# Performance work log

Measured on AMD Instinct MI355X. Metric: run time of the kernel, lower is better.

## Reference

```python
import jax, jax.numpy as jnp
import numpy as np

DIM = 256
HEADS = 8
B, T, D, H, W = 2, 8, 16, 16, 16


def _mha(x, wqkv, bqkv, wo, bo):
    # x: [M, S, F]; standard self-attention (q=k=v=x), LoRA rank 0.
    M, S, F = x.shape
    hd = F // HEADS
    qkv = jnp.einsum('msf,kfg->kmsg', x, wqkv) + bqkv[:, None, None, :]  # [3,M,S,F]
    q, k, v = qkv
    q = q.reshape(M, S, HEADS, hd).transpose(0, 2, 1, 3)  # [M,Hh,S,hd]
    k = k.reshape(M, S, HEADS, hd).transpose(0, 2, 1, 3)
    v = v.reshape(M, S, HEADS, hd).transpose(0, 2, 1, 3)
    scores = jnp.einsum('mhsd,mhtd->mhst', q, k) / jnp.sqrt(jnp.asarray(hd, x.dtype))
    attn = jax.nn.softmax(scores, axis=-1)
    out = jnp.einsum('mhst,mhtd->mhsd', attn, v)
    out = out.transpose(0, 2, 1, 3).reshape(M, S, F)
    return out @ wo + bo


def _make_params(key, name_suffix):
    k1, k2 = jax.random.split(key)
    s = 1.0 / np.sqrt(DIM)
    return {
        f'wqkv_{name_suffix}': jax.random.normal(k1, (3, DIM, DIM), jnp.float32) * s,
        f'bqkv_{name_suffix}': jnp.zeros((3, DIM), jnp.float32),
        f'wo_{name_suffix}': jax.random.normal(k2, (DIM, DIM), jnp.float32) * s,
        f'bo_{name_suffix}': jnp.zeros((DIM,), jnp.float32),
    }


def setup_inputs() -> dict:
    key = jax.random.key(0)
    ks = jax.random.split(key, 5)
    inp = {'x': jax.random.normal(ks[0], (B, T, D * H * W, DIM), jnp.float32)}
    for k, ax in zip(ks[1:], ['t', 'd', 'h', 'w']):
        inp.update(_make_params(k, ax))
    inp['grid_d'] = D
    inp['grid_h'] = H
    inp['grid_w'] = W
    return inp


def reference(x, wqkv_t, bqkv_t, wo_t, bo_t,
              wqkv_d, bqkv_d, wo_d, bo_d,
              wqkv_h, bqkv_h, wo_h, bo_h,
              wqkv_w, bqkv_w, wo_w, bo_w,
              grid_d, grid_h, grid_w):
    b, t, n, f = x.shape
    d, h, w = grid_d, grid_h, grid_w
    x = x.reshape(b, t, d, h, w, f)
    if t > 1:
        xt = x.transpose(0, 2, 3, 4, 1, 5).reshape(b * d * h * w, t, f)
        xt = _mha(xt, wqkv_t, bqkv_t, wo_t, bo_t)
        xt = xt.reshape(b, d, h, w, t, f).transpose(0, 4, 1, 2, 3, 5)
        x = x + xt
    xd = x.transpose(0, 1, 3, 4, 2, 5).reshape(b * t * h * w, d, f)
    xd = _mha(xd, wqkv_d, bqkv_d, wo_d, bo_d)
    xd = xd.reshape(b, t, h, w, d, f).transpose(0, 1, 4, 2, 3, 5)
    xh = x.transpose(0, 1, 2, 4, 3, 5).reshape(b * t * d * w, h, f)
    xh = _mha(xh, wqkv_h, bqkv_h, wo_h, bo_h)
    xh = xh.reshape(b, t, d, w, h, f).transpose(0, 1, 2, 4, 3, 5)
    xw = x.reshape(b * t * d * h, w, f)
    xw = _mha(xw, wqkv_w, bqkv_w, wo_w, bo_w)
    xw = xw.reshape(b, t, d, h, w, f)
    x_comb = x + xd + xh + xw
    return x_comb.reshape(b, t, d * h * w, f)
```

## Files before the change

### kernel.cpp

```cpp
#include <hip/hip_runtime.h>

typedef __attribute__((ext_vector_type(4))) float f32x4;
typedef __attribute__((ext_vector_type(8))) short s16x8;

__device__ __forceinline__ ushort f2bf(float f) {
  union { float f; uint u; } v; v.f = f;
  uint r = v.u + 0x7fffu + ((v.u >> 16) & 1u);
  return (ushort)(r >> 16);
}

__device__ __forceinline__ void glds16(const void* g, void* l) {
  __builtin_amdgcn_global_load_lds(
      (const __attribute__((address_space(1))) uint*)g,
      (__attribute__((address_space(3))) uint*)l, 16, 0, 0);
}

__device__ __forceinline__ int asidx(int row, int col) {
  return row*256 + ((((col>>3) ^ (row & 7)))<<3) + (col&7);
}
__device__ __forceinline__ int scridx(int row, int col) {
  return row*32 + ((((col>>3) ^ ((row>>2)&3)))<<3) + (col&7);
}
__device__ __forceinline__ int epidx(int row, int f) {
  return row*256 + (f ^ ((row & 7) << 2));
}

struct WSrc { const float* p[8]; };

__global__ __launch_bounds__(256) void prep_weights(WSrc s, ushort* wq, ushort* wo) {
  int mm = blockIdx.x >> 6;
  int t  = blockIdx.x & 63;
  int a = mm >> 2, sub = mm & 3;
  const float* src = (sub < 3) ? (s.p[a*2] + sub*65536) : s.p[a*2+1];
  ushort*      dst = (sub < 3) ? (wq + (a*3 + sub)*65536) : (wo + a*65536);
  int gt = (t >> 3) * 32, ft = (t & 7) * 32;
  __shared__ float tile[32][33];
  int lx = threadIdx.x & 31, ly = threadIdx.x >> 5;
#pragma unroll
  for (int i = 0; i < 4; i++)
    tile[ly + i*8][lx] = src[(ft + ly + i*8)*256 + gt + lx];
  __syncthreads();
#pragma unroll
  for (int i = 0; i < 4; i++) {
    int n = gt + ly + i*8, col = ft + lx;
    dst[asidx(n, col)] = f2bf(tile[lx][ly + i*8]);
  }
}

template<int AXIS>
__device__ __forceinline__ int token_index(int blk, int row) {
  if (AXIS == 0) {
    int seq = blk*8 + (row >> 3);
    int t = row & 7;
    int b = seq >> 12, n = seq & 4095;
    return (b*8 + t)*4096 + n;
  } else {
    int sid = blk*4 + (row >> 4);
    int bt = sid >> 8, lo = sid & 255, r = row & 15;
    if (AXIS == 1) { int hh = lo >> 4, ww = lo & 15; return bt*4096 + r*256 + hh*16 + ww; }
    if (AXIS == 2) { int dd = lo >> 4, ww = lo & 15; return bt*4096 + dd*256 + r*16 + ww; }
    { int dd = lo >> 4, hh = lo & 15; return bt*4096 + dd*256 + hh*16 + r; }
  }
}

#define PUB_BARRIER() do { \
    __builtin_amdgcn_sched_barrier(0); \
    asm volatile("s_waitcnt lgkmcnt(0)" ::: "memory"); \
    __builtin_amdgcn_sched_barrier(0); \
    __builtin_amdgcn_s_barrier(); \
    __builtin_amdgcn_sched_barrier(0); } while (0)

template<int AXIS>
__global__ __launch_bounds__(512, 4) void axial_pass(
    const float* __restrict__ x0, const ushort* __restrict__ xb,
    const ushort* __restrict__ wqkvT, const float* __restrict__ bqkv,
    const ushort* __restrict__ woT, const float* __restrict__ bo,
    float* __restrict__ out, ushort* __restrict__ x1b) {

  __shared__ ushort smem[40960];
  ushort* Wb0 = smem;
  ushort* Wb1 = smem + 8192;
  ushort* As  = smem + 16384;
  ushort* ScrB = smem + 32768;

  const int tid = threadIdx.x, blk = blockIdx.x;
  const int wv = tid >> 6, lane = tid & 63, llo = lane & 15, lhi = lane >> 4;
  const int pr = wv >> 1, half = wv & 1;
  const int rr = half*16 + llo;
  ushort* Qs = ScrB + pr*2048;
  ushort* Ks = Qs + 512;
  ushort* Vt = Qs + 1024;
  const f32x4 fzero = {0.f, 0.f, 0.f, 0.f};
  const s16x8 szero = {0,0,0,0,0,0,0,0};

  auto issue_stage = [&](int s) {
    const ushort* src = (s < 24) ? (wqkvT + (s % 3)*65536 + (s / 3)*8192)
                                 : (woT + (s - 24)*8192);
    const ushort* g = src + wv*1024 + lane*8;
    ushort* l = ((s & 1) ? Wb1 : Wb0) + wv*1024;
    glds16(g, l);
    glds16(g + 512, l + 512);
  };

#define STAGE_SYNC(sn) do { \
    __builtin_amdgcn_sched_barrier(0); \
    asm volatile("s_waitcnt vmcnt(0) lgkmcnt(0)" ::: "memory"); \
    __builtin_amdgcn_sched_barrier(0); \
    __builtin_amdgcn_s_barrier(); \
    __builtin_amdgcn_sched_barrier(0); \
    if ((sn) < 32) issue_stage(sn); \
  } while (0)

  issue_stage(0);

  {
    int row = tid >> 3, j = tid & 7;
    int tok = token_index<AXIS>(blk, row);
    if (AXIS == 0) {
      const float4* s4 = (const float4*)(x0 + (size_t)tok*256);
#pragma unroll
      for (int i = 0; i < 4; i++) {
        int c = j + 8*i;
        float4 v0 = s4[c*2], v1 = s4[c*2 + 1];
        s16x8 o;
        o[0] = (short)f2bf(v0.x); o[1] = (short)f2bf(v0.y);
        o[2] = (short)f2bf(v0.z); o[3] = (short)f2bf(v0.w);
        o[4] = (short)f2bf(v1.x); o[5] = (short)f2bf(v1.y);
        o[6] = (short)f2bf(v1.z); o[7] = (short)f2bf(v1.w);
        *(s16x8*)(As + asidx(row, c*8)) = o;
      }
    } else {
      const s16x8* s8 = (const s16x8*)(xb + (size_t)tok*256);
#pragma unroll
      for (int i = 0; i < 4; i++) {
        int c = j + 8*i;
        *(s16x8*)(As + asidx(row, c*8)) = s8[c];
      }
    }
  }
  {
    int row = half*16 + (lane >> 2);
    int cc = 2 + (lane & 1);
    *(s16x8*)(Vt + row*32 + ((cc ^ ((row>>2)&3))<<3)) = szero;
  }
  __syncthreads();

  s16x8 af[8];
  const int xrow = pr*16 + llo;
#pragma unroll
  for (int ks = 0; ks < 8; ks++)
    af[ks] = *(const s16x8*)(As + asidx(xrow, (ks*4 + lhi)*8));

  auto proj = [&](int sb) -> f32x4 {
    const ushort* buf = sb ? Wb1 : Wb0;
    f32x4 ca = fzero, cb = fzero;
    __builtin_amdgcn_s_setprio(1);
#pragma unroll
    for (int ks = 0; ks < 4; ks++) {
      s16x8 b0 = *(const s16x8*)(buf + asidx(rr, (ks*4 + lhi)*8));
      s16x8 b1 = *(const s16x8*)(buf + asidx(rr, ((ks+4)*4 + lhi)*8));
      ca = __builtin_amdgcn_mfma_f32_16x16x32_bf16(af[ks],   b0, ca, 0, 0, 0);
      cb = __builtin_amdgcn_mfma_f32_16x16x32_bf16(af[ks+4], b1, cb, 0, 0, 0);
    }
    __builtin_amdgcn_s_setprio(0);
    return ca + cb;
  };

#pragma unroll 1
  for (int h = 0; h < 8; h++) {
    STAGE_SYNC(3*h + 1);
    {
      f32x4 c = proj((3*h) & 1);
      float bias = bqkv[0*256 + h*32 + rr];
#pragma unroll
      for (int r = 0; r < 4; r++)
        Qs[scridx(lhi*4 + r, rr)] = f2bf(c[r] + bias);
    }
    STAGE_SYNC(3*h + 2);
    {
      f32x4 c = proj((3*h + 1) & 1);
      float bias = bqkv[1*256 + h*32 + rr];
#pragma unroll
      for (int r = 0; r < 4; r++)
        Ks[scridx(lhi*4 + r, rr)] = f2bf(c[r] + bias);
    }
    STAGE_SYNC(3*h + 3);
    {
      f32x4 c = proj((3*h + 2) & 1);
      float bias = bqkv[2*256 + h*32 + rr];
#pragma unroll
      for (int r = 0; r < 4; r++)
        Vt[scridx(rr, lhi*4 + r)] = f2bf(c[r] + bias);

      s16x8 aq = *(const s16x8*)(Qs + scridx(llo, lhi*8));
      s16x8 bk = *(const s16x8*)(Ks + scridx(llo, lhi*8));
      f32x4 sc = __builtin_amdgcn_mfma_f32_16x16x32_bf16(aq, bk, fzero, 0, 0, 0);

      PUB_BARRIER();

#pragma unroll
      for (int r = 0; r < 4; r++) {
        float s = sc[r] * 0.17677669529663689f;
        if (AXIS == 0) {
          int srow = lhi*4 + r;
          if ((srow >> 3) != (llo >> 3)) s = -1e30f;
        }
        float mx = s;
        mx = fmaxf(mx, __shfl_xor(mx, 1));
        mx = fmaxf(mx, __shfl_xor(mx, 2));
        mx = fmaxf(mx, __shfl_xor(mx, 4));
        mx = fmaxf(mx, __shfl_xor(mx, 8));
        float e = __expf(s - mx);
        float sm = e;
        sm += __shfl_xor(sm, 1);
        sm += __shfl_xor(sm, 2);
        sm += __shfl_xor(sm, 4);
        sm += __shfl_xor(sm, 8);
        Ks[scridx(lhi*4 + r, llo)] = f2bf(e * __builtin_amdgcn_rcpf(sm));
      }
      s16x8 ap = *(const s16x8*)(Ks + scridx(llo, lhi*8));
      s16x8 bv = *(const s16x8*)(Vt + scridx(rr, lhi*8));
      f32x4 o = __builtin_amdgcn_mfma_f32_16x16x32_bf16(ap, bv, fzero, 0, 0, 0);
#pragma unroll
      for (int r = 0; r < 4; r++)
        As[asidx(pr*16 + lhi*4 + r, h*32 + rr)] = f2bf(o[r]);
    }
  }

  f32x4 acc[8];
#pragma unroll 1
  for (int st = 0; st < 8; st++) {
    STAGE_SYNC(25 + st);
    if (st == 0) {
#pragma unroll
      for (int ks = 0; ks < 8; ks++)
        af[ks] = *(const s16x8*)(As + asidx(xrow, (ks*4 + lhi)*8));
#pragma unroll
      for (int i = 0; i < 8; i++) acc[i] = fzero;
    }
    {
      const ushort* buf = (st & 1) ? Wb1 : Wb0;
      f32x4 t0 = fzero;
      __builtin_amdgcn_s_setprio(1);
#pragma unroll
      for (int ks = 0; ks < 4; ks++) {
        s16x8 b0 = *(const s16x8*)(buf + asidx(rr, (ks*4 + lhi)*8));
        s16x8 b1 = *(const s16x8*)(buf + asidx(rr, ((ks+4)*4 + lhi)*8));
        acc[st] = __builtin_amdgcn_mfma_f32_16x16x32_bf16(af[ks],   b0, acc[st], 0, 0, 0);
        t0      = __builtin_amdgcn_mfma_f32_16x16x32_bf16(af[ks+4], b1, t0,      0, 0, 0);
      }
      __builtin_amdgcn_s_setprio(0);
      acc[st] = acc[st] + t0;
    }
  }

  float* Fep = (float*)smem;
  PUB_BARRIER();
#pragma unroll
  for (int st = 0; st < 8; st++) {
#pragma unroll
    for (int r = 0; r < 4; r++) {
      int row = pr*16 + lhi*4 + r;
      Fep[epidx(row, st*32 + half*16 + llo)] = acc[st][r];
    }
  }
  PUB_BARRIER();
  {
    int row = tid >> 3, g = tid & 7;
    int tok = token_index<AXIS>(blk, row);
    size_t base = (size_t)tok*256;
#pragma unroll
    for (int i = 0; i < 8; i++) {
      int f = i*32 + g*4;
      float4 v = *(float4*)&Fep[epidx(row, f)];
      float4 b = *(const float4*)&bo[f];
      v.x += b.x; v.y += b.y; v.z += b.z; v.w += b.w;
      if (AXIS == 0) {
        float4 x = *(const float4*)&x0[base + f];
        v.x += x.x; v.y += x.y; v.z += x.z; v.w += x.w;
        *(float4*)&out[base + f] = v;
        ushort4 p; p.x = f2bf(v.x); p.y = f2bf(v.y);
        p.z = f2bf(v.z); p.w = f2bf(v.w);
        *(ushort4*)&x1b[base + f] = p;
      } else {
        float4 o = *(float4*)&out[base + f];
        o.x += v.x; o.y += v.y; o.z += v.z; o.w += v.w;
        *(float4*)&out[base + f] = o;
      }
    }
  }
#undef STAGE_SYNC
}

extern "C" void kernel_launch(void* const* d_in, const int* in_sizes, int n_in,
                              void* d_out, int out_size, void* d_ws, size_t ws_size,
                              hipStream_t stream) {
  const float* x = (const float*)d_in[0];
  ushort* wq  = (ushort*)d_ws;
  ushort* wo  = wq + 4*3*65536;
  ushort* x1b = wo + 4*65536;
  float* out = (float*)d_out;

  WSrc wsrc;
  wsrc.p[0] = (const float*)d_in[1];  wsrc.p[1] = (const float*)d_in[3];
  wsrc.p[2] = (const float*)d_in[5];  wsrc.p[3] = (const float*)d_in[7];
  wsrc.p[4] = (const float*)d_in[9];  wsrc.p[5] = (const float*)d_in[11];
  wsrc.p[6] = (const float*)d_in[13]; wsrc.p[7] = (const float*)d_in[15];
  prep_weights<<<dim3(1024), dim3(256), 0, stream>>>(wsrc, wq, wo);

  const float* bq_t = (const float*)d_in[2];  const float* bo_t = (const float*)d_in[4];
  const float* bq_d = (const float*)d_in[6];  const float* bo_d = (const float*)d_in[8];
  const float* bq_h = (const float*)d_in[10]; const float* bo_h = (const float*)d_in[12];
  const float* bq_w = (const float*)d_in[14]; const float* bo_w = (const float*)d_in[16];

  axial_pass<0><<<dim3(1024), dim3(512), 0, stream>>>(x, nullptr, wq + 0*3*65536, bq_t, wo + 0*65536, bo_t, out, x1b);
  axial_pass<1><<<dim3(1024), dim3(512), 0, stream>>>(nullptr, x1b, wq + 1*3*65536, bq_d, wo + 1*65536, bo_d, out, nullptr);
  axial_pass<2><<<dim3(1024), dim3(512), 0, stream>>>(nullptr, x1b, wq + 2*3*65536, bq_h, wo + 2*65536, bo_h, out, nullptr);
  axial_pass<3><<<dim3(1024), dim3(512), 0, stream>>>(nullptr, x1b, wq + 3*3*65536, bq_w, wo + 3*65536, bo_w, out, nullptr);
}
```

Baseline: 402.8 us.

## Halve block to 256 threads, each wave computing two row groups

```diff
diff --git a/kernel.cpp b/kernel.cpp
--- a/kernel.cpp
+++ b/kernel.cpp
@@ -71,7 +71,7 @@
     __builtin_amdgcn_sched_barrier(0); } while (0)
 
 template<int AXIS>
-__global__ __launch_bounds__(512, 4) void axial_pass(
+__global__ __launch_bounds__(256, 2) void axial_pass(
     const float* __restrict__ x0, const ushort* __restrict__ xb,
     const ushort* __restrict__ wqkvT, const float* __restrict__ bqkv,
     const ushort* __restrict__ woT, const float* __restrict__ bo,
@@ -80,26 +80,22 @@
   __shared__ ushort smem[40960];
   ushort* Wb0 = smem;
   ushort* Wb1 = smem + 8192;
-  ushort* As  = smem + 16384;
-  ushort* ScrB = smem + 32768;
+  ushort* AsT = smem + 16384;
+  ushort* Scr = smem + 32768;
 
   const int tid = threadIdx.x, blk = blockIdx.x;
   const int wv = tid >> 6, lane = tid & 63, llo = lane & 15, lhi = lane >> 4;
-  const int pr = wv >> 1, half = wv & 1;
-  const int rr = half*16 + llo;
-  ushort* Qs = ScrB + pr*2048;
-  ushort* Ks = Qs + 512;
-  ushort* Vt = Qs + 1024;
+  const int rg = wv >> 1, ch = wv & 1;
   const f32x4 fzero = {0.f, 0.f, 0.f, 0.f};
   const s16x8 szero = {0,0,0,0,0,0,0,0};
 
   auto issue_stage = [&](int s) {
     const ushort* src = (s < 24) ? (wqkvT + (s % 3)*65536 + (s / 3)*8192)
                                  : (woT + (s - 24)*8192);
-    const ushort* g = src + wv*1024 + lane*8;
-    ushort* l = ((s & 1) ? Wb1 : Wb0) + wv*1024;
-    glds16(g, l);
-    glds16(g + 512, l + 512);
+    const ushort* g = src + wv*2048 + lane*8;
+    ushort* l = ((s & 1) ? Wb1 : Wb0) + wv*2048;
+#pragma unroll
+    for (int i = 0; i < 4; i++) glds16(g + i*512, l + i*512);
   };
 
 #define STAGE_SYNC(sn) do { \
@@ -114,144 +110,156 @@
   issue_stage(0);
 
   {
-    int row = tid >> 3, j = tid & 7;
+    int row = tid >> 2, q = tid & 3;
     int tok = token_index<AXIS>(blk, row);
     if (AXIS == 0) {
-      const float4* s4 = (const float4*)(x0 + (size_t)tok*256);
-#pragma unroll
-      for (int i = 0; i < 4; i++) {
-        int c = j + 8*i;
-        float4 v0 = s4[c*2], v1 = s4[c*2 + 1];
+      const float4* s4 = (const float4*)(x0 + (size_t)tok*256 + q*64);
+#pragma unroll
+      for (int c2 = 0; c2 < 8; c2++) {
+        float4 v0 = s4[c2*2], v1 = s4[c2*2 + 1];
         s16x8 o;
         o[0] = (short)f2bf(v0.x); o[1] = (short)f2bf(v0.y);
         o[2] = (short)f2bf(v0.z); o[3] = (short)f2bf(v0.w);
         o[4] = (short)f2bf(v1.x); o[5] = (short)f2bf(v1.y);
         o[6] = (short)f2bf(v1.z); o[7] = (short)f2bf(v1.w);
-        *(s16x8*)(As + asidx(row, c*8)) = o;
+        *(s16x8*)(AsT + asidx(row, (q*8 + c2)*8)) = o;
       }
     } else {
-      const s16x8* s8 = (const s16x8*)(xb + (size_t)tok*256);
-#pragma unroll
-      for (int i = 0; i < 4; i++) {
-        int c = j + 8*i;
-        *(s16x8*)(As + asidx(row, c*8)) = s8[c];
-      }
+      const s16x8* s8 = (const s16x8*)(xb + (size_t)tok*256 + q*64);
+#pragma unroll
+      for (int c2 = 0; c2 < 8; c2++)
+        *(s16x8*)(AsT + asidx(row, (q*8 + c2)*8)) = s8[c2];
     }
   }
   {
-    int row = half*16 + (lane >> 2);
-    int cc = 2 + (lane & 1);
-    *(s16x8*)(Vt + row*32 + ((cc ^ ((row>>2)&3))<<3)) = szero;
+    ushort* Vtw = Scr + wv*2048 + 1024;
+    *(s16x8*)(Vtw + scridx(lane >> 1, 16 + (lane & 1)*8)) = szero;
   }
   __syncthreads();
 
-  s16x8 af[8];
-  const int xrow = pr*16 + llo;
-#pragma unroll
-  for (int ks = 0; ks < 8; ks++)
-    af[ks] = *(const s16x8*)(As + asidx(xrow, (ks*4 + lhi)*8));
-
-  auto proj = [&](int sb) -> f32x4 {
+  s16x8 af[2][8];
+#pragma unroll
+  for (int g = 0; g < 2; g++)
+#pragma unroll
+    for (int ks = 0; ks < 8; ks++)
+      af[g][ks] = *(const s16x8*)(AsT + asidx(rg*32 + g*16 + llo, (ks*4 + lhi)*8));
+
+  auto proj2 = [&](int sb, f32x4& c0, f32x4& c1) {
     const ushort* buf = sb ? Wb1 : Wb0;
-    f32x4 ca = fzero, cb = fzero;
     __builtin_amdgcn_s_setprio(1);
 #pragma unroll
-    for (int ks = 0; ks < 4; ks++) {
-      s16x8 b0 = *(const s16x8*)(buf + asidx(rr, (ks*4 + lhi)*8));
-      s16x8 b1 = *(const s16x8*)(buf + asidx(rr, ((ks+4)*4 + lhi)*8));
-      ca = __builtin_amdgcn_mfma_f32_16x16x32_bf16(af[ks],   b0, ca, 0, 0, 0);
-      cb = __builtin_amdgcn_mfma_f32_16x16x32_bf16(af[ks+4], b1, cb, 0, 0, 0);
+    for (int ks = 0; ks < 8; ks++) {
+      s16x8 bv = *(const s16x8*)(buf + asidx(ch*16 + llo, (ks*4 + lhi)*8));
+      c0 = __builtin_amdgcn_mfma_f32_16x16x32_bf16(af[0][ks], bv, c0, 0, 0, 0);
+      c1 = __builtin_amdgcn_mfma_f32_16x16x32_bf16(af[1][ks], bv, c1, 0, 0, 0);
     }
     __builtin_amdgcn_s_setprio(0);
-    return ca + cb;
   };
 
 #pragma unroll 1
   for (int h = 0; h < 8; h++) {
     STAGE_SYNC(3*h + 1);
     {
-      f32x4 c = proj((3*h) & 1);
-      float bias = bqkv[0*256 + h*32 + rr];
-#pragma unroll
-      for (int r = 0; r < 4; r++)
-        Qs[scridx(lhi*4 + r, rr)] = f2bf(c[r] + bias);
+      f32x4 c0 = fzero, c1 = fzero;
+      proj2((3*h) & 1, c0, c1);
+      float bi = bqkv[h*32 + ch*16 + llo];
+      ushort* q0 = Scr + (rg*2 + 0)*2048;
+      ushort* q1 = Scr + (rg*2 + 1)*2048;
+#pragma unroll
+      for (int r = 0; r < 4; r++) {
+        q0[scridx(lhi*4 + r, ch*16 + llo)] = f2bf(c0[r] + bi);
+        q1[scridx(lhi*4 + r, ch*16 + llo)] = f2bf(c1[r] + bi);
+      }
     }
     STAGE_SYNC(3*h + 2);
     {
-      f32x4 c = proj((3*h + 1) & 1);
-      float bias = bqkv[1*256 + h*32 + rr];
-#pragma unroll
-      for (int r = 0; r < 4; r++)
-        Ks[scridx(lhi*4 + r, rr)] = f2bf(c[r] + bias);
+      f32x4 c0 = fzero, c1 = fzero;
+      proj2((3*h + 1) & 1, c0, c1);
+      float bi = bqkv[256 + h*32 + ch*16 + llo];
+      ushort* k0 = Scr + (rg*2 + 0)*2048 + 512;
+      ushort* k1 = Scr + (rg*2 + 1)*2048 + 512;
+#pragma unroll
+      for (int r = 0; r < 4; r++) {
+        k0[scridx(lhi*4 + r, ch*16 + llo)] = f2bf(c0[r] + bi);
+        k1[scridx(lhi*4 + r, ch*16 + llo)] = f2bf(c1[r] + bi);
+      }
     }
     STAGE_SYNC(3*h + 3);
     {
-      f32x4 c = proj((3*h + 2) & 1);
-      float bias = bqkv[2*256 + h*32 + rr];
-#pragma unroll
-      for (int r = 0; r < 4; r++)
-        Vt[scridx(rr, lhi*4 + r)] = f2bf(c[r] + bias);
-
-      s16x8 aq = *(const s16x8*)(Qs + scridx(llo, lhi*8));
-      s16x8 bk = *(const s16x8*)(Ks + scridx(llo, lhi*8));
+      f32x4 c0 = fzero, c1 = fzero;
+      proj2((3*h + 2) & 1, c0, c1);
+      float bi = bqkv[512 + h*32 + ch*16 + llo];
+      ushort* v0 = Scr + (rg*2 + 0)*2048 + 1024;
+      ushort* v1 = Scr + (rg*2 + 1)*2048 + 1024;
+#pragma unroll
+      for (int r = 0; r < 4; r++) {
+        v0[scridx(ch*16 + llo, lhi*4 + r)] = f2bf(c0[r] + bi);
+        v1[scridx(ch*16 + llo, lhi*4 + r)] = f2bf(c1[r] + bi);
+      }
+    }
+    PUB_BARRIER();
+
+    {
+      ushort* S = Scr + wv*2048;
+      s16x8 aq = *(const s16x8*)(S + scridx(llo, lhi*8));
+      s16x8 bk = *(const s16x8*)(S + 512 + scridx(llo, lhi*8));
       f32x4 sc = __builtin_amdgcn_mfma_f32_16x16x32_bf16(aq, bk, fzero, 0, 0, 0);
-
-      PUB_BARRIER();
-
-#pragma unroll
-      for (int r = 0; r < 4; r++) {
-        float s = sc[r] * 0.17677669529663689f;
+#pragma unroll
+      for (int r = 0; r < 4; r++) {
+        float sv = sc[r] * 0.17677669529663689f;
         if (AXIS == 0) {
           int srow = lhi*4 + r;
-          if ((srow >> 3) != (llo >> 3)) s = -1e30f;
+          if ((srow >> 3) != (llo >> 3)) sv = -1e30f;
         }
-        float mx = s;
+        float mx = sv;
         mx = fmaxf(mx, __shfl_xor(mx, 1));
         mx = fmaxf(mx, __shfl_xor(mx, 2));
         mx = fmaxf(mx, __shfl_xor(mx, 4));
         mx = fmaxf(mx, __shfl_xor(mx, 8));
-        float e = __expf(s - mx);
+        float e = __expf(sv - mx);
         float sm = e;
         sm += __shfl_xor(sm, 1);
         sm += __shfl_xor(sm, 2);
         sm += __shfl_xor(sm, 4);
         sm += __shfl_xor(sm, 8);
-        Ks[scridx(lhi*4 + r, llo)] = f2bf(e * __builtin_amdgcn_rcpf(sm));
-      }
-      s16x8 ap = *(const s16x8*)(Ks + scridx(llo, lhi*8));
-      s16x8 bv = *(const s16x8*)(Vt + scridx(rr, lhi*8));
-      f32x4 o = __builtin_amdgcn_mfma_f32_16x16x32_bf16(ap, bv, fzero, 0, 0, 0);
-#pragma unroll
-      for (int r = 0; r < 4; r++)
-        As[asidx(pr*16 + lhi*4 + r, h*32 + rr)] = f2bf(o[r]);
-    }
-  }
-
-  f32x4 acc[8];
+        (S + 512)[scridx(lhi*4 + r, llo)] = f2bf(e * __builtin_amdgcn_rcpf(sm));
+      }
+      s16x8 ap  = *(const s16x8*)(S + 512 + scridx(llo, lhi*8));
+      s16x8 bv0 = *(const s16x8*)(S + 1024 + scridx(llo, lhi*8));
+      s16x8 bv1 = *(const s16x8*)(S + 1024 + scridx(16 + llo, lhi*8));
+      f32x4 o0 = __builtin_amdgcn_mfma_f32_16x16x32_bf16(ap, bv0, fzero, 0, 0, 0);
+      f32x4 o1 = __builtin_amdgcn_mfma_f32_16x16x32_bf16(ap, bv1, fzero, 0, 0, 0);
+#pragma unroll
+      for (int r = 0; r < 4; r++) {
+        AsT[asidx(wv*16 + lhi*4 + r, h*32 + llo)]      = f2bf(o0[r]);
+        AsT[asidx(wv*16 + lhi*4 + r, h*32 + 16 + llo)] = f2bf(o1[r]);
+      }
+    }
+  }
+
+  PUB_BARRIER();
+
+#pragma unroll
+  for (int g = 0; g < 2; g++)
+#pragma unroll
+    for (int ks = 0; ks < 8; ks++)
+      af[g][ks] = *(const s16x8*)(AsT + asidx(rg*32 + g*16 + llo, (ks*4 + lhi)*8));
+
+  f32x4 acc[16];
+#pragma unroll
+  for (int i = 0; i < 16; i++) acc[i] = fzero;
 #pragma unroll 1
   for (int st = 0; st < 8; st++) {
     STAGE_SYNC(25 + st);
-    if (st == 0) {
-#pragma unroll
-      for (int ks = 0; ks < 8; ks++)
-        af[ks] = *(const s16x8*)(As + asidx(xrow, (ks*4 + lhi)*8));
-#pragma unroll
-      for (int i = 0; i < 8; i++) acc[i] = fzero;
-    }
-    {
-      const ushort* buf = (st & 1) ? Wb1 : Wb0;
-      f32x4 t0 = fzero;
-      __builtin_amdgcn_s_setprio(1);
-#pragma unroll
-      for (int ks = 0; ks < 4; ks++) {
-        s16x8 b0 = *(const s16x8*)(buf + asidx(rr, (ks*4 + lhi)*8));
-        s16x8 b1 = *(const s16x8*)(buf + asidx(rr, ((ks+4)*4 + lhi)*8));
-        acc[st] = __builtin_amdgcn_mfma_f32_16x16x32_bf16(af[ks],   b0, acc[st], 0, 0, 0);
-        t0      = __builtin_amdgcn_mfma_f32_16x16x32_bf16(af[ks+4], b1, t0,      0, 0, 0);
-      }
-      __builtin_amdgcn_s_setprio(0);
-      acc[st] = acc[st] + t0;
-    }
+    const ushort* buf = (st & 1) ? Wb1 : Wb0;
+    __builtin_amdgcn_s_setprio(1);
+#pragma unroll
+    for (int ks = 0; ks < 8; ks++) {
+      s16x8 bv = *(const s16x8*)(buf + asidx(ch*16 + llo, (ks*4 + lhi)*8));
+      acc[st*2]   = __builtin_amdgcn_mfma_f32_16x16x32_bf16(af[0][ks], bv, acc[st*2],   0, 0, 0);
+      acc[st*2+1] = __builtin_amdgcn_mfma_f32_16x16x32_bf16(af[1][ks], bv, acc[st*2+1], 0, 0, 0);
+    }
+    __builtin_amdgcn_s_setprio(0);
   }
 
   float* Fep = (float*)smem;
@@ -259,33 +267,40 @@
 #pragma unroll
   for (int st = 0; st < 8; st++) {
 #pragma unroll
-    for (int r = 0; r < 4; r++) {
-      int row = pr*16 + lhi*4 + r;
-      Fep[epidx(row, st*32 + half*16 + llo)] = acc[st][r];
+    for (int g = 0; g < 2; g++) {
+#pragma unroll
+      for (int r = 0; r < 4; r++) {
+        int row = rg*32 + g*16 + lhi*4 + r;
+        Fep[epidx(row, st*32 + ch*16 + llo)] = acc[st*2 + g][r];
+      }
     }
   }
   PUB_BARRIER();
   {
-    int row = tid >> 3, g = tid & 7;
-    int tok = token_index<AXIS>(blk, row);
-    size_t base = (size_t)tok*256;
-#pragma unroll
-    for (int i = 0; i < 8; i++) {
-      int f = i*32 + g*4;
-      float4 v = *(float4*)&Fep[epidx(row, f)];
-      float4 b = *(const float4*)&bo[f];
-      v.x += b.x; v.y += b.y; v.z += b.z; v.w += b.w;
-      if (AXIS == 0) {
-        float4 x = *(const float4*)&x0[base + f];
-        v.x += x.x; v.y += x.y; v.z += x.z; v.w += x.w;
-        *(float4*)&out[base + f] = v;
-        ushort4 p; p.x = f2bf(v.x); p.y = f2bf(v.y);
-        p.z = f2bf(v.z); p.w = f2bf(v.w);
-        *(ushort4*)&x1b[base + f] = p;
-      } else {
-        float4 o = *(float4*)&out[base + f];
-        o.x += v.x; o.y += v.y; o.z += v.z; o.w += v.w;
-        *(float4*)&out[base + f] = o;
+    int rbase = tid >> 3, g = tid & 7;
+#pragma unroll 1
+    for (int step = 0; step < 2; step++) {
+      int row = rbase + step*32;
+      int tok = token_index<AXIS>(blk, row);
+      size_t base = (size_t)tok*256;
+#pragma unroll
+      for (int i = 0; i < 8; i++) {
+        int f = i*32 + g*4;
+        float4 v = *(float4*)&Fep[epidx(row, f)];
+        float4 b = *(const float4*)&bo[f];
+        v.x += b.x; v.y += b.y; v.z += b.z; v.w += b.w;
+        if (AXIS == 0) {
+          float4 x = *(const float4*)&x0[base + f];
+          v.x += x.x; v.y += x.y; v.z += x.z; v.w += x.w;
+          *(float4*)&out[base + f] = v;
+          ushort4 p; p.x = f2bf(v.x); p.y = f2bf(v.y);
+          p.z = f2bf(v.z); p.w = f2bf(v.w);
+          *(ushort4*)&x1b[base + f] = p;
+        } else {
+          float4 o = *(float4*)&out[base + f];
+          o.x += v.x; o.y += v.y; o.z += v.z; o.w += v.w;
+          *(float4*)&out[base + f] = o;
+        }
       }
     }
   }
@@ -313,8 +328,8 @@
   const float* bq_h = (const float*)d_in[10]; const float* bo_h = (const float*)d_in[12];
   const float* bq_w = (const float*)d_in[14]; const float* bo_w = (const float*)d_in[16];
 
-  axial_pass<0><<<dim3(1024), dim3(512), 0, stream>>>(x, nullptr, wq + 0*3*65536, bq_t, wo + 0*65536, bo_t, out, x1b);
-  axial_pass<1><<<dim3(1024), dim3(512), 0, stream>>>(nullptr, x1b, wq + 1*3*65536, bq_d, wo + 1*65536, bo_d, out, nullptr);
-  axial_pass<2><<<dim3(1024), dim3(512), 0, stream>>>(nullptr, x1b, wq + 2*3*65536, bq_h, wo + 2*65536, bo_h, out, nullptr);
-  axial_pass<3><<<dim3(1024), dim3(512), 0, stream>>>(nullptr, x1b, wq + 3*3*65536, bq_w, wo + 3*65536, bo_w, out, nullptr);
-}
+  axial_pass<0><<<dim3(1024), dim3(256), 0, stream>>>(x, nullptr, wq + 0*3*65536, bq_t, wo + 0*65536, bo_t, out, x1b);
+  axial_pass<1><<<dim3(1024), dim3(256), 0, stream>>>(nullptr, x1b, wq + 1*3*65536, bq_d, wo + 1*65536, bo_d, out, nullptr);
+  axial_pass<2><<<dim3(1024), dim3(256), 0, stream>>>(nullptr, x1b, wq + 2*3*65536, bq_h, wo + 2*65536, bo_h, out, nullptr);
+  axial_pass<3><<<dim3(1024), dim3(256), 0, stream>>>(nullptr, x1b, wq + 3*3*65536, bq_w, wo + 3*65536, bo_w, out, nullptr);
+}
```

Measured after the change: 462.6 us. 14.8% more time.
